# Kernel optimization log

Measured on AMD Instinct MI355X. Metric: run time of the kernel, lower is better.

## Reference

```python
import jax, jax.numpy as jnp
import numpy as np
import math

D_MODEL = 1024
NUM_HEADS = 16
D_KV = 64
INNER = NUM_HEADS * D_KV
NUM_BUCKETS = 32
MAX_DISTANCE = 128


def _relative_position_bucket(relative_position, num_buckets=NUM_BUCKETS, max_distance=MAX_DISTANCE):
    # bidirectional T5 bucketing
    n = -relative_position
    num_buckets = num_buckets // 2
    ret = (n < 0).astype(jnp.int32) * num_buckets
    n = jnp.abs(n)
    max_exact = num_buckets // 2
    is_small = n < max_exact
    n_safe = jnp.maximum(n, 1).astype(jnp.float32)  # avoid log(0); masked by is_small
    val_if_large = max_exact + (
        jnp.log(n_safe / max_exact) / math.log(max_distance / max_exact) * (num_buckets - max_exact)
    ).astype(jnp.int32)
    val_if_large = jnp.minimum(val_if_large, num_buckets - 1)
    return jnp.where(is_small, n, val_if_large) + ret


def _position_bias(rel_emb, q_len, k_len):
    ctx = jnp.arange(q_len)[:, None]
    mem = jnp.arange(k_len)[None, :]
    buckets = _relative_position_bucket(mem - ctx)          # [q, k]
    values = rel_emb[buckets]                               # [q, k, H]
    return jnp.transpose(values, (2, 0, 1))[None]           # [1, H, q, k]


def setup_inputs() -> dict:
    key = jax.random.key(0)
    ks = jax.random.split(key, 6)
    B, S = 2, 2048
    scale = 1.0 / math.sqrt(D_MODEL)
    return {
        "hidden_states": jax.random.normal(ks[0], (B, S, D_MODEL), dtype=jnp.float32),
        "mask": jnp.zeros((B, 1, 1, S), dtype=jnp.float32),
        "Wq": jax.random.normal(ks[1], (D_MODEL, INNER), dtype=jnp.float32) * scale,
        "Wk": jax.random.normal(ks[2], (D_MODEL, INNER), dtype=jnp.float32) * scale,
        "Wv": jax.random.normal(ks[3], (D_MODEL, INNER), dtype=jnp.float32) * scale,
        "Wo": jax.random.normal(ks[4], (INNER, D_MODEL), dtype=jnp.float32) * scale,
        "rel_emb": jax.random.normal(ks[5], (NUM_BUCKETS, NUM_HEADS), dtype=jnp.float32),
    }


def reference(hidden_states, mask, Wq, Wk, Wv, Wo, rel_emb):
    B, S, _ = hidden_states.shape
    def split_heads(x):
        return jnp.transpose(x.reshape(B, -1, NUM_HEADS, D_KV), (0, 2, 1, 3))  # [B,H,S,d]
    q = split_heads(hidden_states @ Wq)
    k = split_heads(hidden_states @ Wk)
    v = split_heads(hidden_states @ Wv)
    scores = jnp.einsum("bhqd,bhkd->bhqk", q, k)            # unscaled, T5-style
    position_bias = _position_bias(rel_emb, S, S)           # [1,H,S,S]
    scores = scores + position_bias + mask
    attn = jax.nn.softmax(scores, axis=-1)
    context = jnp.einsum("bhqk,bhkd->bhqd", attn, v)
    context = jnp.transpose(context, (0, 2, 1, 3)).reshape(B, S, INNER)
    output = context @ Wo
    return output, position_bias
```

## Files before the change

kernel.cpp:

```cpp
#include <hip/hip_runtime.h>
#include <cstdint>

#define AS1 __attribute__((address_space(1)))
#define AS3 __attribute__((address_space(3)))

typedef _Float16 half8 __attribute__((ext_vector_type(8)));
typedef _Float16 half4_t __attribute__((ext_vector_type(4)));
typedef float v4f __attribute__((ext_vector_type(4)));

__device__ __forceinline__ void async_ld16(const void* g, void* l) {
  __builtin_amdgcn_global_load_lds((const AS1 uint32_t*)g, (AS3 uint32_t*)l, 16, 0, 0);
}

__device__ __forceinline__ int t5_bucket(int delta) {
  int n = -delta;
  int ret = 0;
  if (n < 0) { ret = 16; n = -n; }
  if (n < 8) return n + ret;
  if (n >= 91) return 15 + ret;
  if ((n & (n - 1)) == 0) {
    int l = 31 - __clz(n);
    int v = 2 + 2 * l;
    return (v > 15 ? 15 : v) + ret;
  }
  int v = 8 + (int)(logf((float)n * 0.125f) * (8.0f / logf(16.0f)));
  return (v > 15 ? 15 : v) + ret;
}

__global__ void k_prep(const float* __restrict__ hs, const float* __restrict__ Wq,
                       const float* __restrict__ Wk, const float* __restrict__ Wv,
                       const float* __restrict__ Wo, _Float16* __restrict__ hsF,
                       _Float16* __restrict__ wqkvT, _Float16* __restrict__ woT) {
  const int tid = threadIdx.x;
  if (blockIdx.x < 4096) {
    int t = blockIdx.x * 256 + tid;
    float4 f = ((const float4*)hs)[t];
    half4_t h = {(_Float16)f.x, (_Float16)f.y, (_Float16)f.z, (_Float16)f.w};
    ((half4_t*)hsF)[t] = h;
    return;
  }
  __shared__ float tile[32][33];
  const int idx = blockIdx.x - 4096;
  const int z = idx >> 10, rem = idx & 1023;
  const float* src = (z == 0) ? Wq : (z == 1) ? Wk : (z == 2) ? Wv : Wo;
  _Float16* dst = (z < 3) ? (wqkvT + ((size_t)z << 20)) : woT;
  const int tx = tid & 31, ty = tid >> 5;
  const int bx = (rem & 31) * 32, by = (rem >> 5) * 32;
#pragma unroll
  for (int i = 0; i < 32; i += 8)
    tile[ty + i][tx] = src[(size_t)(by + ty + i) * 1024 + bx + tx];
  __syncthreads();
#pragma unroll
  for (int i = 0; i < 32; i += 8)
    dst[(size_t)(bx + ty + i) * 1024 + by + tx] = (_Float16)tile[tx][ty + i];
}

__global__ __launch_bounds__(256, 2) void k_gemm_qkv_bias(
    const _Float16* __restrict__ A, const _Float16* __restrict__ BT,
    _Float16* __restrict__ qkv, _Float16* __restrict__ vT,
    const float* __restrict__ rel, float* __restrict__ outb) {
  __shared__ __align__(16) _Float16 As[128 * 32];
  __shared__ __align__(16) _Float16 Bs[128 * 32];
  __shared__ float btab[256];
  const int tid = threadIdx.x;
  const int wave = tid >> 6, lane = tid & 63;
  const int l15 = lane & 15, quad = lane >> 4;
  const int m0 = blockIdx.y * 128, n0 = blockIdx.x * 128;
  const int wm = (wave >> 1) * 64, wn = (wave & 1) * 64;
  const int r0 = tid >> 2, c0 = (tid & 3) * 8;
  constexpr int K = 1024;

  const int bid = blockIdx.y * 24 + blockIdx.x;
  const bool do_bias = bid < 512;
  const int hB = bid >> 5;
  const int qoff = (bid & 31) * 64;
  float c_past = 0.f, c_fut = 0.f;
  if (do_bias) {
    btab[tid & 255] = rel[t5_bucket((tid & 255) - 128) * 16 + hB];
    c_past = rel[15 * 16 + hB];
    c_fut = rel[31 * 16 + hB];
  }

  v4f acc[4][4] = {};
  for (int k0 = 0; k0 < K; k0 += 32) {
    __syncthreads();
    async_ld16(A + (size_t)(m0 + r0) * K + k0 + c0, (char*)As + (size_t)(wave * 64) * 16);
    async_ld16(A + (size_t)(m0 + 64 + r0) * K + k0 + c0,
               (char*)As + (size_t)(256 + wave * 64) * 16);
    async_ld16(BT + (size_t)(n0 + r0) * K + k0 + c0, (char*)Bs + (size_t)(wave * 64) * 16);
    async_ld16(BT + (size_t)(n0 + 64 + r0) * K + k0 + c0,
               (char*)Bs + (size_t)(256 + wave * 64) * 16);
    __syncthreads();

    if (do_bias) {
      const int iter = k0 >> 5;
#pragma unroll
      for (int j = 0; j < 4; ++j) {
        int fi = iter * 1024 + j * 256 + tid;
        int qr = qoff + (fi >> 9);
        int kb = (fi & 511) * 4;
        float4 v;
        if (kb - qr >= 91) {
          v = make_float4(c_fut, c_fut, c_fut, c_fut);
        } else if (qr - kb - 3 >= 91) {
          v = make_float4(c_past, c_past, c_past, c_past);
        } else {
          v.x = btab[kb + 0 - qr + 128];
          v.y = btab[kb + 1 - qr + 128];
          v.z = btab[kb + 2 - qr + 128];
          v.w = btab[kb + 3 - qr + 128];
        }
        ((float4*)outb)[(size_t)bid * 32768 + fi] = v;
      }
    }

    half8 af[4], bf[4];
#pragma unroll
    for (int mt = 0; mt < 4; ++mt)
      af[mt] = *(const half8*)(As + (wm + mt * 16 + l15) * 32 + quad * 8);
#pragma unroll
    for (int nt = 0; nt < 4; ++nt)
      bf[nt] = *(const half8*)(Bs + (wn + nt * 16 + l15) * 32 + quad * 8);
#pragma unroll
    for (int mt = 0; mt < 4; ++mt)
#pragma unroll
      for (int nt = 0; nt < 4; ++nt)
        acc[mt][nt] = __builtin_amdgcn_mfma_f32_16x16x32_f16(af[mt], bf[nt], acc[mt][nt], 0, 0, 0);
  }
  if (n0 >= 2048) {
#pragma unroll
    for (int mt = 0; mt < 4; ++mt)
#pragma unroll
      for (int nt = 0; nt < 4; ++nt) {
        int col = n0 + wn + nt * 16 + l15 - 2048;
        int row0 = m0 + wm + mt * 16 + quad * 4;
        int bb = row0 >> 11, s0 = row0 & 2047;
        half4_t hv = {(_Float16)acc[mt][nt][0], (_Float16)acc[mt][nt][1],
                      (_Float16)acc[mt][nt][2], (_Float16)acc[mt][nt][3]};
        *(half4_t*)(vT + ((size_t)bb * 1024 + col) * 2048 + s0) = hv;
      }
    return;
  }
#pragma unroll
  for (int mt = 0; mt < 4; ++mt)
#pragma unroll
    for (int nt = 0; nt < 4; ++nt)
#pragma unroll
      for (int r = 0; r < 4; ++r)
        qkv[(size_t)(m0 + wm + mt * 16 + quad * 4 + r) * 3072 + n0 + wn + nt * 16 + l15] =
            (_Float16)acc[mt][nt][r];
}

__global__ __launch_bounds__(256, 2) void k_gemm_n64(const _Float16* __restrict__ A,
                                                     const _Float16* __restrict__ BT,
                                                     float* __restrict__ C, int K, int ldc) {
  __shared__ __align__(16) _Float16 As[128 * 32];
  __shared__ __align__(16) _Float16 Bs[64 * 32];
  const int tid = threadIdx.x;
  const int wave = tid >> 6, lane = tid & 63;
  const int l15 = lane & 15, quad = lane >> 4;
  const int m0 = blockIdx.y * 128, n0 = blockIdx.x * 64;
  const int wm = (wave >> 1) * 64, wn = (wave & 1) * 32;
  const int r0 = tid >> 2, c0 = (tid & 3) * 8;
  v4f acc[4][2] = {};
  for (int k0 = 0; k0 < K; k0 += 32) {
    __syncthreads();
    async_ld16(A + (size_t)(m0 + r0) * K + k0 + c0, (char*)As + (size_t)(wave * 64) * 16);
    async_ld16(A + (size_t)(m0 + 64 + r0) * K + k0 + c0,
               (char*)As + (size_t)(256 + wave * 64) * 16);
    async_ld16(BT + (size_t)(n0 + r0) * K + k0 + c0, (char*)Bs + (size_t)(wave * 64) * 16);
    __syncthreads();
    half8 af[4], bf[2];
#pragma unroll
    for (int mt = 0; mt < 4; ++mt)
      af[mt] = *(const half8*)(As + (wm + mt * 16 + l15) * 32 + quad * 8);
#pragma unroll
    for (int nt = 0; nt < 2; ++nt)
      bf[nt] = *(const half8*)(Bs + (wn + nt * 16 + l15) * 32 + quad * 8);
#pragma unroll
    for (int mt = 0; mt < 4; ++mt)
#pragma unroll
      for (int nt = 0; nt < 2; ++nt)
        acc[mt][nt] = __builtin_amdgcn_mfma_f32_16x16x32_f16(af[mt], bf[nt], acc[mt][nt], 0, 0, 0);
  }
#pragma unroll
  for (int mt = 0; mt < 4; ++mt)
#pragma unroll
    for (int nt = 0; nt < 2; ++nt)
#pragma unroll
      for (int r = 0; r < 4; ++r)
        C[(size_t)(m0 + wm + mt * 16 + quad * 4 + r) * ldc + n0 + wn + nt * 16 + l15] =
            acc[mt][nt][r];
}

__global__ __launch_bounds__(256, 2) void k_attn(const _Float16* __restrict__ qkv,
                                                 const _Float16* __restrict__ vT,
                                                 const float* __restrict__ mask,
                                                 const float* __restrict__ rel,
                                                 _Float16* __restrict__ ctx) {
  constexpr int S = 2048, LD = 3072;
  __shared__ __align__(16) _Float16 Ks[2][64 * 72];
  __shared__ __align__(16) _Float16 VT[2][64 * 72];
  __shared__ __align__(16) _Float16 Psh[128 * 72];
  __shared__ float btab[512];
  const int tid = threadIdx.x, wave = tid >> 6, lane = tid & 63;
  const int l15 = lane & 15, quad = lane >> 4;
  const int q0 = blockIdx.x * 128, h = blockIdx.y, b = blockIdx.z;

  for (int j = tid; j < 512; j += 256) btab[j] = rel[t5_bucket(j - 256) * 16 + h];
  const float c_past = rel[15 * 16 + h];
  const float c_fut = rel[31 * 16 + h];

  half8 bq[2][2];
#pragma unroll
  for (int qt = 0; qt < 2; ++qt) {
    const _Float16* qp = qkv + (size_t)(b * S + q0 + wave * 32 + qt * 16 + l15) * LD + h * 64;
    bq[qt][0] = *(const half8*)(qp + quad * 8);
    bq[qt][1] = *(const half8*)(qp + 32 + quad * 8);
  }
  v4f o[2][4] = {};
  float mrun[2] = {-INFINITY, -INFINITY};
  float lrun[2] = {0.f, 0.f};

  const int srow = tid >> 2, scol = (tid & 3) * 8;
  const _Float16* kg = qkv + (size_t)(b * S + srow) * LD + 1024 + h * 64 + scol;
  const _Float16* vg = vT + ((size_t)((b * 16 + h) * 64 + srow)) * S + scol;
  const float4* mkp = (const float4*)(mask + (size_t)b * S);

  {
    half8 kr0 = *(const half8*)(kg);
    half8 kr1 = *(const half8*)(kg + 32);
    half8 vr0 = *(const half8*)(vg);
    half8 vr1 = *(const half8*)(vg + 32);
    *(half8*)(&Ks[0][srow * 72 + scol]) = kr0;
    *(half8*)(&Ks[0][srow * 72 + scol + 32]) = kr1;
    *(half8*)(&VT[0][srow * 72 + scol]) = vr0;
    *(half8*)(&VT[0][srow * 72 + scol + 32]) = vr1;
  }
  float4 mk[4];
#pragma unroll
  for (int mt = 0; mt < 4; ++mt) mk[mt] = mkp[mt * 4 + quad];
  __syncthreads();

  for (int kv0 = 0; kv0 < S; kv0 += 64) {
    const int buf = (kv0 >> 6) & 1;
    const bool more = (kv0 + 64) < S;
    half8 kr0n, kr1n, vr0n, vr1n;
    float4 mkn[4];
    if (more) {
      kr0n = *(const half8*)(kg + (size_t)(kv0 + 64) * LD);
      kr1n = *(const half8*)(kg + (size_t)(kv0 + 64) * LD + 32);
      vr0n = *(const half8*)(vg + kv0 + 64);
      vr1n = *(const half8*)(vg + kv0 + 64 + 32);
#pragma unroll
      for (int mt = 0; mt < 4; ++mt) mkn[mt] = mkp[((kv0 + 64) >> 2) + mt * 4 + quad];
    }

    const _Float16* KsB = &Ks[buf][0];
    const _Float16* VTB = &VT[buf][0];
    v4f sc[2][4] = {};
#pragma unroll
    for (int kc = 0; kc < 2; ++kc)
#pragma unroll
      for (int mt = 0; mt < 4; ++mt) {
        half8 af = *(const half8*)(KsB + (mt * 16 + l15) * 72 + kc * 32 + quad * 8);
        sc[0][mt] = __builtin_amdgcn_mfma_f32_16x16x32_f16(af, bq[0][kc], sc[0][mt], 0, 0, 0);
        sc[1][mt] = __builtin_amdgcn_mfma_f32_16x16x32_f16(af, bq[1][kc], sc[1][mt], 0, 0, 0);
      }

    const int diff = kv0 - q0;
    const bool mixed = (diff >= -153) && (diff <= 217);
    const float cf = (diff >= 218) ? c_fut : c_past;
    v4f cm[4];
#pragma unroll
    for (int mt = 0; mt < 4; ++mt) {
      cm[mt][0] = mk[mt].x; cm[mt][1] = mk[mt].y; cm[mt][2] = mk[mt].z; cm[mt][3] = mk[mt].w;
      if (!mixed) {
        cm[mt][0] += cf; cm[mt][1] += cf; cm[mt][2] += cf; cm[mt][3] += cf;
      }
    }
    if (mixed) {
#pragma unroll
      for (int qt = 0; qt < 2; ++qt) {
        const int qq = q0 + wave * 32 + qt * 16 + l15;
#pragma unroll
        for (int mt = 0; mt < 4; ++mt) {
          int base = kv0 + mt * 16 + quad * 4 - qq + 256;
#pragma unroll
          for (int r = 0; r < 4; ++r) sc[qt][mt][r] += btab[base + r] + cm[mt][r];
        }
      }
    } else {
#pragma unroll
      for (int qt = 0; qt < 2; ++qt)
#pragma unroll
        for (int mt = 0; mt < 4; ++mt)
#pragma unroll
          for (int r = 0; r < 4; ++r) sc[qt][mt][r] += cm[mt][r];
    }

#pragma unroll
    for (int qt = 0; qt < 2; ++qt) {
      v4f m4 = sc[qt][0];
#pragma unroll
      for (int r = 0; r < 4; ++r) {
        m4[r] = fmaxf(m4[r], sc[qt][1][r]);
        m4[r] = fmaxf(m4[r], sc[qt][2][r]);
        m4[r] = fmaxf(m4[r], sc[qt][3][r]);
      }
      float mx = fmaxf(fmaxf(m4[0], m4[1]), fmaxf(m4[2], m4[3]));
      mx = fmaxf(mx, __shfl_xor(mx, 16, 64));
      mx = fmaxf(mx, __shfl_xor(mx, 32, 64));
      float mnew = fmaxf(mrun[qt], mx);
      float alpha = __expf(mrun[qt] - mnew);
      mrun[qt] = mnew;
      v4f s4 = {};
#pragma unroll
      for (int mt = 0; mt < 4; ++mt)
#pragma unroll
        for (int r = 0; r < 4; ++r) {
          float p = __expf(sc[qt][mt][r] - mnew);
          sc[qt][mt][r] = p;
          s4[r] += p;
        }
      float rs = (s4[0] + s4[1]) + (s4[2] + s4[3]);
      rs += __shfl_xor(rs, 16, 64);
      rs += __shfl_xor(rs, 32, 64);
      lrun[qt] = lrun[qt] * alpha + rs;
#pragma unroll
      for (int dt = 0; dt < 4; ++dt)
#pragma unroll
        for (int r = 0; r < 4; ++r) o[qt][dt][r] *= alpha;
      const int prow = wave * 32 + qt * 16 + l15;
#pragma unroll
      for (int mt = 0; mt < 4; ++mt) {
        half4_t ph = {(_Float16)sc[qt][mt][0], (_Float16)sc[qt][mt][1],
                      (_Float16)sc[qt][mt][2], (_Float16)sc[qt][mt][3]};
        *(half4_t*)(Psh + prow * 72 + mt * 16 + quad * 4) = ph;
      }
    }

#pragma unroll
    for (int kc = 0; kc < 2; ++kc) {
      half8 bp0 = *(const half8*)(Psh + (wave * 32 + l15) * 72 + kc * 32 + quad * 8);
      half8 bp1 = *(const half8*)(Psh + (wave * 32 + 16 + l15) * 72 + kc * 32 + quad * 8);
#pragma unroll
      for (int dt = 0; dt < 4; ++dt) {
        half8 av = *(const half8*)(VTB + (dt * 16 + l15) * 72 + kc * 32 + quad * 8);
        o[0][dt] = __builtin_amdgcn_mfma_f32_16x16x32_f16(av, bp0, o[0][dt], 0, 0, 0);
        o[1][dt] = __builtin_amdgcn_mfma_f32_16x16x32_f16(av, bp1, o[1][dt], 0, 0, 0);
      }
    }

    if (more) {
      _Float16* Kn = &Ks[buf ^ 1][0];
      _Float16* Vn = &VT[buf ^ 1][0];
      *(half8*)(Kn + srow * 72 + scol) = kr0n;
      *(half8*)(Kn + srow * 72 + scol + 32) = kr1n;
      *(half8*)(Vn + srow * 72 + scol) = vr0n;
      *(half8*)(Vn + srow * 72 + scol + 32) = vr1n;
      __syncthreads();
#pragma unroll
      for (int mt = 0; mt < 4; ++mt) mk[mt] = mkn[mt];
    }
  }
#pragma unroll
  for (int qt = 0; qt < 2; ++qt) {
    float inv = 1.0f / lrun[qt];
    const size_t token = (size_t)(b * S + q0 + wave * 32 + qt * 16 + l15);
#pragma unroll
    for (int dt = 0; dt < 4; ++dt) {
      half4_t hv = {(_Float16)(o[qt][dt][0] * inv), (_Float16)(o[qt][dt][1] * inv),
                    (_Float16)(o[qt][dt][2] * inv), (_Float16)(o[qt][dt][3] * inv)};
      *(half4_t*)(ctx + token * 1024 + h * 64 + dt * 16 + quad * 4) = hv;
    }
  }
}

extern "C" void kernel_launch(void* const* d_in, const int* in_sizes, int n_in,
                              void* d_out, int out_size, void* d_ws, size_t ws_size,
                              hipStream_t stream) {
  const float* hs = (const float*)d_in[0];
  const float* mask = (const float*)d_in[1];
  const float* Wq = (const float*)d_in[2];
  const float* Wk = (const float*)d_in[3];
  const float* Wv = (const float*)d_in[4];
  const float* Wo = (const float*)d_in[5];
  const float* rel = (const float*)d_in[6];
  float* out = (float*)d_out;

  char* ws = (char*)d_ws;
  _Float16* hsF = (_Float16*)(ws);
  _Float16* wqkvT = (_Float16*)(ws + (8u << 20));
  _Float16* woT = (_Float16*)(ws + (14u << 20));
  _Float16* qkv = (_Float16*)(ws + (16u << 20));
  _Float16* ctx = (_Float16*)(ws + (40u << 20));
  _Float16* vT = (_Float16*)(ws + (48u << 20));

  k_prep<<<8192, 256, 0, stream>>>(hs, Wq, Wk, Wv, Wo, hsF, wqkvT, woT);

  k_gemm_qkv_bias<<<dim3(24, 32), 256, 0, stream>>>(hsF, wqkvT, qkv, vT, rel,
                                                    out + 4194304);
  k_attn<<<dim3(16, 16, 2), 256, 0, stream>>>(qkv, vT, mask, rel, ctx);
  k_gemm_n64<<<dim3(16, 32), 256, 0, stream>>>(ctx, woT, out, 1024, 1024);
}
```

Before: 425.0 us.

## Swizzle attention LDS tiles, drop padding, and raise occupancy target to three blocks

```diff
diff --git a/kernel.cpp b/kernel.cpp
--- a/kernel.cpp
+++ b/kernel.cpp
@@ -10,6 +10,11 @@
 
 __device__ __forceinline__ void async_ld16(const void* g, void* l) {
   __builtin_amdgcn_global_load_lds((const AS1 uint32_t*)g, (AS3 uint32_t*)l, 16, 0, 0);
+}
+
+__device__ __forceinline__ int sw(int row, int col_half) {
+  int chunk = col_half >> 3, rem = col_half & 7;
+  return row * 64 + (((chunk ^ (row & 7)) << 3) | rem);
 }
 
 __device__ __forceinline__ int t5_bucket(int delta) {
@@ -55,7 +60,7 @@
     dst[(size_t)(bx + ty + i) * 1024 + by + tx] = (_Float16)tile[tx][ty + i];
 }
 
-__global__ __launch_bounds__(256, 2) void k_gemm_qkv_bias(
+__global__ __launch_bounds__(256, 3) void k_gemm_qkv_bias(
     const _Float16* __restrict__ A, const _Float16* __restrict__ BT,
     _Float16* __restrict__ qkv, _Float16* __restrict__ vT,
     const float* __restrict__ rel, float* __restrict__ outb) {
@@ -193,15 +198,15 @@
             acc[mt][nt][r];
 }
 
-__global__ __launch_bounds__(256, 2) void k_attn(const _Float16* __restrict__ qkv,
+__global__ __launch_bounds__(256, 3) void k_attn(const _Float16* __restrict__ qkv,
                                                  const _Float16* __restrict__ vT,
                                                  const float* __restrict__ mask,
                                                  const float* __restrict__ rel,
                                                  _Float16* __restrict__ ctx) {
   constexpr int S = 2048, LD = 3072;
-  __shared__ __align__(16) _Float16 Ks[2][64 * 72];
-  __shared__ __align__(16) _Float16 VT[2][64 * 72];
-  __shared__ __align__(16) _Float16 Psh[128 * 72];
+  __shared__ __align__(16) _Float16 Ks[2][64 * 64];
+  __shared__ __align__(16) _Float16 VT[2][64 * 64];
+  __shared__ __align__(16) _Float16 Psh[128 * 64];
   __shared__ float btab[512];
   const int tid = threadIdx.x, wave = tid >> 6, lane = tid & 63;
   const int l15 = lane & 15, quad = lane >> 4;
@@ -232,29 +237,26 @@
     half8 kr1 = *(const half8*)(kg + 32);
     half8 vr0 = *(const half8*)(vg);
     half8 vr1 = *(const half8*)(vg + 32);
-    *(half8*)(&Ks[0][srow * 72 + scol]) = kr0;
-    *(half8*)(&Ks[0][srow * 72 + scol + 32]) = kr1;
-    *(half8*)(&VT[0][srow * 72 + scol]) = vr0;
-    *(half8*)(&VT[0][srow * 72 + scol + 32]) = vr1;
-  }
-  float4 mk[4];
-#pragma unroll
-  for (int mt = 0; mt < 4; ++mt) mk[mt] = mkp[mt * 4 + quad];
+    *(half8*)(&Ks[0][sw(srow, scol)]) = kr0;
+    *(half8*)(&Ks[0][sw(srow, scol + 32)]) = kr1;
+    *(half8*)(&VT[0][sw(srow, scol)]) = vr0;
+    *(half8*)(&VT[0][sw(srow, scol + 32)]) = vr1;
+  }
   __syncthreads();
 
   for (int kv0 = 0; kv0 < S; kv0 += 64) {
     const int buf = (kv0 >> 6) & 1;
     const bool more = (kv0 + 64) < S;
     half8 kr0n, kr1n, vr0n, vr1n;
-    float4 mkn[4];
     if (more) {
       kr0n = *(const half8*)(kg + (size_t)(kv0 + 64) * LD);
       kr1n = *(const half8*)(kg + (size_t)(kv0 + 64) * LD + 32);
       vr0n = *(const half8*)(vg + kv0 + 64);
       vr1n = *(const half8*)(vg + kv0 + 64 + 32);
-#pragma unroll
-      for (int mt = 0; mt < 4; ++mt) mkn[mt] = mkp[((kv0 + 64) >> 2) + mt * 4 + quad];
-    }
+    }
+    float4 mk[4];
+#pragma unroll
+    for (int mt = 0; mt < 4; ++mt) mk[mt] = mkp[(kv0 >> 2) + mt * 4 + quad];
 
     const _Float16* KsB = &Ks[buf][0];
     const _Float16* VTB = &VT[buf][0];
@@ -263,7 +265,7 @@
     for (int kc = 0; kc < 2; ++kc)
 #pragma unroll
       for (int mt = 0; mt < 4; ++mt) {
-        half8 af = *(const half8*)(KsB + (mt * 16 + l15) * 72 + kc * 32 + quad * 8);
+        half8 af = *(const half8*)(KsB + sw(mt * 16 + l15, kc * 32 + quad * 8));
         sc[0][mt] = __builtin_amdgcn_mfma_f32_16x16x32_f16(af, bq[0][kc], sc[0][mt], 0, 0, 0);
         sc[1][mt] = __builtin_amdgcn_mfma_f32_16x16x32_f16(af, bq[1][kc], sc[1][mt], 0, 0, 0);
       }
@@ -336,17 +338,17 @@
       for (int mt = 0; mt < 4; ++mt) {
         half4_t ph = {(_Float16)sc[qt][mt][0], (_Float16)sc[qt][mt][1],
                       (_Float16)sc[qt][mt][2], (_Float16)sc[qt][mt][3]};
-        *(half4_t*)(Psh + prow * 72 + mt * 16 + quad * 4) = ph;
+        *(half4_t*)(&Psh[sw(prow, mt * 16 + quad * 4)]) = ph;
       }
     }
 
 #pragma unroll
     for (int kc = 0; kc < 2; ++kc) {
-      half8 bp0 = *(const half8*)(Psh + (wave * 32 + l15) * 72 + kc * 32 + quad * 8);
-      half8 bp1 = *(const half8*)(Psh + (wave * 32 + 16 + l15) * 72 + kc * 32 + quad * 8);
+      half8 bp0 = *(const half8*)(&Psh[sw(wave * 32 + l15, kc * 32 + quad * 8)]);
+      half8 bp1 = *(const half8*)(&Psh[sw(wave * 32 + 16 + l15, kc * 32 + quad * 8)]);
 #pragma unroll
       for (int dt = 0; dt < 4; ++dt) {
-        half8 av = *(const half8*)(VTB + (dt * 16 + l15) * 72 + kc * 32 + quad * 8);
+        half8 av = *(const half8*)(VTB + sw(dt * 16 + l15, kc * 32 + quad * 8));
         o[0][dt] = __builtin_amdgcn_mfma_f32_16x16x32_f16(av, bp0, o[0][dt], 0, 0, 0);
         o[1][dt] = __builtin_amdgcn_mfma_f32_16x16x32_f16(av, bp1, o[1][dt], 0, 0, 0);
       }
@@ -355,13 +357,11 @@
     if (more) {
       _Float16* Kn = &Ks[buf ^ 1][0];
       _Float16* Vn = &VT[buf ^ 1][0];
-      *(half8*)(Kn + srow * 72 + scol) = kr0n;
-      *(half8*)(Kn + srow * 72 + scol + 32) = kr1n;
-      *(half8*)(Vn + srow * 72 + scol) = vr0n;
-      *(half8*)(Vn + srow * 72 + scol + 32) = vr1n;
+      *(half8*)(Kn + sw(srow, scol)) = kr0n;
+      *(half8*)(Kn + sw(srow, scol + 32)) = kr1n;
+      *(half8*)(Vn + sw(srow, scol)) = vr0n;
+      *(half8*)(Vn + sw(srow, scol + 32)) = vr1n;
       __syncthreads();
-#pragma unroll
-      for (int mt = 0; mt < 4; ++mt) mk[mt] = mkn[mt];
     }
   }
 #pragma unroll
```

Result: slower. 437.7 us (+3.0%).
